# Kernel optimization log

Hardware: AMD Instinct MI355X
Metric: run time of the kernel (lower is better)

Reference implementation:

```python
import jax, jax.numpy as jnp
import numpy as np
import math

B, S, D, H = 2, 1024, 1024, 16
DH = D // H
BUCKETS, MAXPOS = 256, 512
SPAN = BUCKETS  # pos_ebd_size (att_span)


def make_log_bucket_position(rel, bucket_size, max_position):
    sign = jnp.sign(rel).astype(jnp.float32)
    mid = bucket_size // 2
    abs_pos = jnp.where((rel < mid) & (rel > -mid), mid - 1, jnp.abs(rel)).astype(jnp.float32)
    log_pos = jnp.ceil(jnp.log(abs_pos / mid) / np.log((max_position - 1) / mid) * (mid - 1)) + mid
    return jnp.where(abs_pos <= mid, rel.astype(jnp.float32), log_pos * sign).astype(jnp.int32)


def build_relative_position(q_size, k_size):
    rel = jnp.arange(q_size, dtype=jnp.int32)[:, None] - jnp.arange(k_size, dtype=jnp.int32)[None, :]
    return make_log_bucket_position(rel, BUCKETS, MAXPOS)


def setup_inputs() -> dict:
    key = jax.random.key(0)
    ks = jax.random.split(key, 8)
    w = lambda k: jax.random.normal(k, (D, D), dtype=jnp.float32) * 0.02
    return {
        "hidden_states": jax.random.normal(ks[0], (B, S, D), dtype=jnp.float32),
        "attention_mask": jnp.ones((B, 1, S, S), dtype=jnp.int32),
        "rel_embeddings": jax.random.normal(ks[1], (2 * SPAN, D), dtype=jnp.float32),
        "Wq": w(ks[2]), "bq": jnp.zeros((D,), jnp.float32),
        "Wk": w(ks[3]), "bk": jnp.zeros((D,), jnp.float32),
        "Wv": w(ks[4]), "bv": jnp.zeros((D,), jnp.float32),
    }


def reference(hidden_states, attention_mask, rel_embeddings, Wq, bq, Wk, bk, Wv, bv):
    split = lambda x: x.reshape(B, -1, H, DH).transpose(0, 2, 1, 3)  # [B,H,S,dh]
    q = split(hidden_states @ Wq + bq)
    k = split(hidden_states @ Wk + bk)
    v = split(hidden_states @ Wv + bv)

    SCALE_FACTOR = 3  # 1 + c2p + p2c
    scale = math.sqrt(DH * SCALE_FACTOR)
    scores = jnp.einsum('bhqd,bhkd->bhqk', q, k) / scale

    # disentangled relative-position bias (share_att_key=True -> reuse q/k proj)
    re = rel_embeddings[: 2 * SPAN]  # [2*SPAN, D]
    pos_q = (re @ Wq + bq).reshape(2 * SPAN, H, DH).transpose(1, 0, 2)  # [H,P,dh]
    pos_k = (re @ Wk + bk).reshape(2 * SPAN, H, DH).transpose(1, 0, 2)

    rel_pos = build_relative_position(S, S)  # [S,S] bucketized

    # c2p: gather along the position axis per (q,k) pair
    c2p_pos = jnp.clip(rel_pos + SPAN, 0, 2 * SPAN - 1)
    c2p_att = jnp.einsum('bhqd,hpd->bhqp', q, pos_k)  # [B,H,S,2*SPAN]
    c2p = jnp.take_along_axis(c2p_att, c2p_pos[None, None], axis=-1)  # [B,H,S,S]

    # p2c: gather for key positions, then transpose back to [q,k]
    p2c_pos = jnp.clip(-rel_pos + SPAN, 0, 2 * SPAN - 1)
    p2c_att = jnp.einsum('bhkd,hpd->bhkp', k, pos_q)
    p2c = jnp.swapaxes(jnp.take_along_axis(p2c_att, p2c_pos[None, None], axis=-1), -1, -2)

    scores = scores + (c2p + p2c) / scale

    # XSoftmax: masked fill -> softmax -> zero masked
    valid = attention_mask.astype(bool)
    scores = jnp.where(valid, scores, jnp.finfo(scores.dtype).min)
    probs = jax.nn.softmax(scores, axis=-1)
    probs = jnp.where(valid, probs, 0.0)

    ctx = jnp.einsum('bhqk,bhkd->bhqd', probs, v)
    return ctx.transpose(0, 2, 1, 3).reshape(B, S, D)
```

## Files before the change

### kernel.cpp

```cpp
#include <hip/hip_runtime.h>
#include <hip/hip_bf16.h>
#include <math.h>

#define B_   2
#define S_   1024
#define D_   1024
#define H_   16
#define DH_  64
#define P_   512

#define SCALE2 (0.07216878364870323f * 1.4426950408889634f)

typedef __bf16 bf16;
typedef __bf16 bf16x8 __attribute__((ext_vector_type(8)));
typedef __bf16 bf16x4 __attribute__((ext_vector_type(4)));
typedef float  f32x4  __attribute__((ext_vector_type(4)));

__device__ __forceinline__ f32x4 mfma16(bf16x8 a, bf16x8 b, f32x4 c) {
  return __builtin_amdgcn_mfma_f32_16x16x32_bf16(a, b, c, 0, 0, 0);
}

__device__ __forceinline__ bf16x8 ld8(const bf16* p) {
  return *reinterpret_cast<const bf16x8*>(p);
}

__device__ __forceinline__ void gl_lds16(const bf16* g, bf16* l) {
  __builtin_amdgcn_global_load_lds(
      (const __attribute__((address_space(1))) void*)g,
      (__attribute__((address_space(3))) void*)l, 16, 0, 0);
}

__device__ __forceinline__ bf16x8 ld8f(const float* p) {
  const f32x4* pv = reinterpret_cast<const f32x4*>(p);
  f32x4 lo = pv[0], hi = pv[1];
  bf16x8 r;
#pragma unroll
  for (int j = 0; j < 4; j++) { r[j] = (bf16)lo[j]; r[4 + j] = (bf16)hi[j]; }
  return r;
}

__global__ __launch_bounds__(256)
void k_convert(const float* __restrict__ hidden, const float* __restrict__ re,
               bf16* __restrict__ Xc, int* __restrict__ ci) {
  int gt = blockIdx.x * 256 + threadIdx.x;
  if (gt < 2047) {
    int rel = gt - 1023;
    int sgn = (rel > 0) - (rel < 0);
    float abs_pos = (rel < 128 && rel > -128) ? 127.0f : fabsf((float)rel);
    int bucket;
    if (abs_pos <= 128.0f) {
      bucket = rel;
    } else {
      const float logden = 1.3843393302355437f;
      float t1 = logf(abs_pos * (1.0f / 128.0f));
      float lp = ceilf(t1 / logden * 127.0f) + 128.0f;
      bucket = (int)lp * sgn;
    }
    ci[gt] = min(max(bucket + 256, 0), 511);
  }
  size_t i8 = (size_t)gt * 8;
  const size_t HN = (size_t)2048 * 1024;
  const float* src = (i8 < HN) ? (hidden + i8) : (re + (i8 - HN));
  *reinterpret_cast<bf16x8*>(&Xc[i8]) = ld8f(src);
}

__global__ __launch_bounds__(256)
void k_transpose(const float* __restrict__ Wq, const float* __restrict__ Wk,
                 const float* __restrict__ Wv, bf16* __restrict__ Wt) {
  __shared__ bf16 tile[64][72];
  const int t = threadIdx.x;
  const int w = blockIdx.z;
  const float* W = (w == 0) ? Wq : (w == 1) ? Wk : Wv;
  bf16* Out = Wt + (size_t)w * D_ * D_;
  const int k0 = blockIdx.y * 64;
  const int n0 = blockIdx.x * 64;
  {
    const int row = t >> 2, c0 = (t & 3) * 16;
    bf16x8 v0 = ld8f(W + (size_t)(k0 + row) * D_ + n0 + c0);
    bf16x8 v1 = ld8f(W + (size_t)(k0 + row) * D_ + n0 + c0 + 8);
    *reinterpret_cast<bf16x8*>(&tile[row][c0]) = v0;
    *reinterpret_cast<bf16x8*>(&tile[row][c0 + 8]) = v1;
  }
  __syncthreads();
  {
    const int nr = t >> 2, kc0 = (t & 3) * 16;
    bf16x8 o0, o1;
#pragma unroll
    for (int j = 0; j < 8; j++) o0[j] = tile[kc0 + j][nr];
#pragma unroll
    for (int j = 0; j < 8; j++) o1[j] = tile[kc0 + 8 + j][nr];
    *reinterpret_cast<bf16x8*>(&Out[(size_t)(n0 + nr) * D_ + k0 + kc0]) = o0;
    *reinterpret_cast<bf16x8*>(&Out[(size_t)(n0 + nr) * D_ + k0 + kc0 + 8]) = o1;
  }
}

__global__ __launch_bounds__(256)
void k_proj(const bf16* __restrict__ Xc, const bf16* __restrict__ Wt,
            const float* __restrict__ bq, const float* __restrict__ bk,
            const float* __restrict__ bv,
            bf16* __restrict__ qb, bf16* __restrict__ kb, bf16* __restrict__ vbT,
            bf16* __restrict__ posq, bf16* __restrict__ posk) {
  __shared__ bf16 As[128 * 64];
  __shared__ bf16 Bs[128 * 64];
  const int t = threadIdx.x;
  const int w = t >> 6, lane = t & 63, quad = lane >> 4, lc = lane & 15;
  const int wm = w >> 1, wn = w & 1;
  const int m0 = blockIdx.y * 128;
  const int wsel = blockIdx.x >> 3;
  const int n0 = (blockIdx.x & 7) * 128;
  const bf16* WtW = Wt + (size_t)wsel * D_ * D_;
  const float* bias = (wsel == 0) ? bq : (wsel == 1) ? bk : bv;
  const bf16* Agl = Xc + (size_t)m0 * D_;
  const bf16* Bgl = WtW + (size_t)n0 * D_;

  int rS[4], cS[4];
#pragma unroll
  for (int i = 0; i < 4; i++) {
    int g = i * 256 + t;
    rS[i] = g >> 3;
    cS[i] = (g & 7) ^ (rS[i] & 7);
  }

  f32x4 zv = {0.f, 0.f, 0.f, 0.f};
  f32x4 acc[4][4];
#pragma unroll
  for (int i = 0; i < 4; i++)
#pragma unroll
    for (int j = 0; j < 4; j++) acc[i][j] = zv;

  for (int k0 = 0; k0 < D_; k0 += 64) {
#pragma unroll
    for (int i = 0; i < 4; i++)
      gl_lds16(Agl + (size_t)rS[i] * D_ + k0 + cS[i] * 8,
               &As[(i * 256 + w * 64) * 8]);
#pragma unroll
    for (int i = 0; i < 4; i++)
      gl_lds16(Bgl + (size_t)rS[i] * D_ + k0 + cS[i] * 8,
               &Bs[(i * 256 + w * 64) * 8]);
    __syncthreads();

#pragma unroll
    for (int h = 0; h < 2; h++) {
      bf16x8 af[4], bfr[4];
#pragma unroll
      for (int mt = 0; mt < 4; mt++) {
        int row = wm * 64 + mt * 16 + lc;
        int ch = (h * 4 + quad) ^ (row & 7);
        af[mt] = ld8(&As[row * 64 + ch * 8]);
      }
#pragma unroll
      for (int nt = 0; nt < 4; nt++) {
        int row = wn * 64 + nt * 16 + lc;
        int ch = (h * 4 + quad) ^ (row & 7);
        bfr[nt] = ld8(&Bs[row * 64 + ch * 8]);
      }
#pragma unroll
      for (int mt = 0; mt < 4; mt++)
#pragma unroll
        for (int nt = 0; nt < 4; nt++)
          acc[mt][nt] = mfma16(af[mt], bfr[nt], acc[mt][nt]);
    }
    __syncthreads();
  }

#pragma unroll
  for (int nt = 0; nt < 4; nt++) {
    int nl = n0 + wn * 64 + nt * 16 + lc;
    float bsv = bias[nl];
    int h = nl >> 6, d = nl & 63;
    if (wsel == 2) {
#pragma unroll
      for (int mt = 0; mt < 4; mt++) {
        int i0 = m0 + wm * 64 + mt * 16 + quad * 4;
        if (i0 < 2048) {
          int b = i0 >> 10, s0 = i0 & 1023;
          bf16x4 ov;
#pragma unroll
          for (int r = 0; r < 4; r++) ov[r] = (bf16)(acc[mt][nt][r] + bsv);
          *reinterpret_cast<bf16x4*>(
              &vbT[(((size_t)(b * H_ + h)) * DH_ + d) * S_ + s0]) = ov;
        }
      }
    } else {
      bf16* dst = (wsel == 0) ? qb : kb;
#pragma unroll
      for (int mt = 0; mt < 4; mt++) {
#pragma unroll
        for (int r = 0; r < 4; r++) {
          int i = m0 + wm * 64 + mt * 16 + quad * 4 + r;
          bf16 ob = (bf16)(acc[mt][nt][r] + bsv);
          if (i < 2048) {
            int b = i >> 10, s = i & 1023;
            dst[(((size_t)(b * H_ + h)) * S_ + s) * DH_ + d] = ob;
          } else {
            int p = i - 2048;
            if (wsel == 0)      posq[((size_t)(h * P_ + p)) * DH_ + d] = ob;
            else                posk[((size_t)(h * P_ + p)) * DH_ + d] = ob;
          }
        }
      }
    }
  }
}

__global__ __launch_bounds__(256)
void k_rel(const bf16* __restrict__ qb, const bf16* __restrict__ kb,
           const bf16* __restrict__ posq, const bf16* __restrict__ posk,
           bf16* __restrict__ c2p, bf16* __restrict__ p2c) {
  const int t = threadIdx.x;
  const int w = t >> 6, lane = t & 63, quad = lane >> 4, lc = lane & 15;
  const int which = blockIdx.z & 1;
  const int bh = blockIdx.z >> 1;
  const int h = bh & (H_ - 1);
  const int q0 = blockIdx.x * 64;
  const bf16* QK = (which ? kb : qb) + (size_t)bh * S_ * DH_;
  const bf16* PM = (which ? posq : posk) + (size_t)h * P_ * DH_;
  bf16* Out = (which ? p2c : c2p) + (size_t)bh * S_ * P_;

  f32x4 zv = {0.f, 0.f, 0.f, 0.f};
  bf16x8 bq[4][2];
#pragma unroll
  for (int qi = 0; qi < 4; qi++) {
    const bf16* qp = QK + (size_t)(q0 + qi * 16 + lc) * DH_ + quad * 8;
    bq[qi][0] = ld8(qp);
    bq[qi][1] = ld8(qp + 32);
  }
  const int p0 = w * 128;
#pragma unroll 2
  for (int pt = 0; pt < 8; pt++) {
    const bf16* pp = PM + (size_t)(p0 + pt * 16 + lc) * DH_ + quad * 8;
    bf16x8 pa0 = ld8(pp), pa1 = ld8(pp + 32);
#pragma unroll
    for (int qi = 0; qi < 4; qi++) {
      f32x4 acc = mfma16(pa1, bq[qi][1], mfma16(pa0, bq[qi][0], zv));
      int q = q0 + qi * 16 + lc;
      int pbase = p0 + pt * 16 + quad * 4;
      bf16x4 ov;
#pragma unroll
      for (int r = 0; r < 4; r++) ov[r] = (bf16)acc[r];
      *reinterpret_cast<bf16x4*>(&Out[(size_t)q * P_ + pbase]) = ov;
    }
  }
}

__global__ __launch_bounds__(256)
void k_attn(const bf16* __restrict__ qb, const bf16* __restrict__ kb,
            const bf16* __restrict__ vbT, const bf16* __restrict__ c2p,
            const bf16* __restrict__ p2c, const int* __restrict__ citab,
            float* __restrict__ out) {
  __shared__ bf16 c2pS[64 * 136];
  __shared__ bf16 p2cS[64 * 136];
  __shared__ bf16 vT[64 * 64];
  __shared__ bf16 Pld[4][16][72];
  __shared__ int  ciS[128];

  const int t = threadIdx.x;
  const int w = t >> 6, lane = t & 63, quad = lane >> 4, lc = lane & 15;
  const int bh = blockIdx.x;
  const int q0 = blockIdx.y * 64;
  const int qw = q0 + w * 16;

  const bf16* qp = qb + ((size_t)bh * S_ + qw + lc) * DH_ + quad * 8;
  bf16x8 aq0 = ld8(qp), aq1 = ld8(qp + 32);

  const bf16* kbB = kb + (size_t)bh * S_ * DH_;
  const bf16* vbB = vbT + (size_t)bh * DH_ * S_;
  const bf16* c2pB = c2p + (size_t)bh * S_ * P_;
  const bf16* p2cB = p2c + (size_t)bh * S_ * P_;

  int wrow[5], wch[5];
#pragma unroll
  for (int i = 0; i < 5; i++) {
    int slot = i * 256 + ((i == 4) ? (t & 63) : t);
    wrow[i] = slot / 17;
    wch[i] = slot - wrow[i] * 17;
  }
  int vrow[2], vch[2];
#pragma unroll
  for (int i = 0; i < 2; i++) {
    int slot = i * 256 + t;
    vrow[i] = slot >> 3;
    vch[i] = (slot & 7) ^ (vrow[i] & 7);
  }

  f32x4 zv = {0.f, 0.f, 0.f, 0.f};
  float m_r[4], l_r[4];
  f32x4 oacc[4];
#pragma unroll
  for (int r = 0; r < 4; r++) { m_r[r] = -INFINITY; l_r[r] = 0.f; }
#pragma unroll
  for (int dg = 0; dg < 4; dg++) oacc[dg] = zv;

  for (int kt = 0; kt < S_; kt += 64) {
    const int clo8 = citab[q0 - kt - 63 + 1023] & ~7;

    bf16x8 kf[4][2];
#pragma unroll
    for (int g = 0; g < 4; g++) {
      const bf16* kp = kbB + (size_t)(kt + g * 16 + lc) * DH_ + quad * 8;
      kf[g][0] = ld8(kp);
      kf[g][1] = ld8(kp + 32);
    }

    if (t < 127) ciS[t] = citab[q0 - kt - 63 + 1023 + t];

#pragma unroll
    for (int i = 0; i < 4; i++) {
      gl_lds16(c2pB + (size_t)(q0 + wrow[i]) * P_ + clo8 + wch[i] * 8,
               &c2pS[(i * 256 + w * 64) * 8]);
      gl_lds16(p2cB + (size_t)(kt + wrow[i]) * P_ + clo8 + wch[i] * 8,
               &p2cS[(i * 256 + w * 64) * 8]);
    }
    if (w == 0) {
      gl_lds16(c2pB + (size_t)(q0 + wrow[4]) * P_ + clo8 + wch[4] * 8,
               &c2pS[1024 * 8]);
      gl_lds16(p2cB + (size_t)(kt + wrow[4]) * P_ + clo8 + wch[4] * 8,
               &p2cS[1024 * 8]);
    }
#pragma unroll
    for (int i = 0; i < 2; i++)
      gl_lds16(vbB + (size_t)vrow[i] * S_ + kt + vch[i] * 8,
               &vT[(i * 256 + w * 64) * 8]);

    f32x4 s[4];
#pragma unroll
    for (int g = 0; g < 4; g++)
      s[g] = mfma16(aq1, kf[g][1], mfma16(aq0, kf[g][0], zv));

    __syncthreads();

#pragma unroll
    for (int g = 0; g < 4; g++) {
      int kc = g * 16 + lc;
#pragma unroll
      for (int r = 0; r < 4; r++) {
        int qr = w * 16 + quad * 4 + r;
        int j = ciS[qr - kc + 63] - clo8;
        float cv = (float)c2pS[qr * 136 + j];
        float pv = (float)p2cS[kc * 136 + j];
        s[g][r] = (s[g][r] + cv + pv) * SCALE2;
      }
    }
#pragma unroll
    for (int r = 0; r < 4; r++) {
      float mx = fmaxf(fmaxf(s[0][r], s[1][r]), fmaxf(s[2][r], s[3][r]));
#pragma unroll
      for (int o2 = 1; o2 < 16; o2 <<= 1) mx = fmaxf(mx, __shfl_xor(mx, o2, 16));
      float mnew = fmaxf(m_r[r], mx);
      float alpha = exp2f(m_r[r] - mnew);
      m_r[r] = mnew;
      float ps = 0.f;
#pragma unroll
      for (int g = 0; g < 4; g++) {
        float pe = exp2f(s[g][r] - mnew);
        s[g][r] = pe;
        ps += pe;
      }
#pragma unroll
      for (int o2 = 1; o2 < 16; o2 <<= 1) ps += __shfl_xor(ps, o2, 16);
      l_r[r] = l_r[r] * alpha + ps;
#pragma unroll
      for (int dg = 0; dg < 4; dg++) oacc[dg][r] *= alpha;
    }
#pragma unroll
    for (int g = 0; g < 4; g++)
#pragma unroll
      for (int r = 0; r < 4; r++)
        Pld[w][quad * 4 + r][g * 16 + lc] = (bf16)s[g][r];

    bf16x8 ap0 = *reinterpret_cast<bf16x8*>(&Pld[w][lc][quad * 8]);
    bf16x8 ap1 = *reinterpret_cast<bf16x8*>(&Pld[w][lc][32 + quad * 8]);
#pragma unroll
    for (int dg = 0; dg < 4; dg++) {
      int row = dg * 16 + lc;
      bf16x8 bv0 = ld8(&vT[row * 64 + (quad ^ (row & 7)) * 8]);
      bf16x8 bv1 = ld8(&vT[row * 64 + ((quad + 4) ^ (row & 7)) * 8]);
      oacc[dg] = mfma16(ap1, bv1, mfma16(ap0, bv0, oacc[dg]));
    }
    __syncthreads();
  }

  const int b = bh >> 4, h = bh & 15;
#pragma unroll
  for (int r = 0; r < 4; r++) {
    float inv = 1.0f / l_r[r];
    int qa = qw + quad * 4 + r;
#pragma unroll
    for (int dg = 0; dg < 4; dg++)
      out[((size_t)(b * S_) + qa) * D_ + h * DH_ + dg * 16 + lc] =
          oacc[dg][r] * inv;
  }
}

extern "C" void kernel_launch(void* const* d_in, const int* in_sizes, int n_in,
                              void* d_out, int out_size, void* d_ws,
                              size_t ws_size, hipStream_t stream) {
  const float* hidden = (const float*)d_in[0];
  const float* re = (const float*)d_in[2];
  const float* Wq = (const float*)d_in[3];
  const float* bq = (const float*)d_in[4];
  const float* Wk = (const float*)d_in[5];
  const float* bk = (const float*)d_in[6];
  const float* Wv = (const float*)d_in[7];
  const float* bv = (const float*)d_in[8];

  char* ws = (char*)d_ws;
  const size_t MB = 1024 * 1024;
  bf16* qb   = (bf16*)(ws + 0 * MB);
  bf16* kb   = (bf16*)(ws + 4 * MB);
  bf16* vbT  = (bf16*)(ws + 8 * MB);
  bf16* posq = (bf16*)(ws + 12 * MB);
  bf16* posk = (bf16*)(ws + 13 * MB);
  int*  ci   = (int*) (ws + 14 * MB);
  bf16* Wt   = (bf16*)(ws + 15 * MB);
  bf16* c2p  = (bf16*)(ws + 26 * MB);
  bf16* p2c  = (bf16*)(ws + 58 * MB);
  bf16* Xc   = (bf16*)(ws + 26 * MB);
  if (ws_size < 92 * MB) return;

  k_convert<<<dim3(1280), dim3(256), 0, stream>>>(hidden, re, Xc, ci);
  k_transpose<<<dim3(16, 16, 3), dim3(256), 0, stream>>>(Wq, Wk, Wv, Wt);
  k_proj<<<dim3(24, 20), dim3(256), 0, stream>>>(Xc, Wt, bq, bk, bv,
                                                 qb, kb, vbT, posq, posk);
  k_rel<<<dim3(16, 1, 64), dim3(256), 0, stream>>>(qb, kb, posq, posk, c2p, p2c);
  k_attn<<<dim3(32, 16), dim3(256), 0, stream>>>(qb, kb, vbT, c2p, p2c, ci,
                                                 (float*)d_out);
}
```

Baseline: 220.6 us.

## Split attention key range across two blocks and merge with combine kernel

The attention kernel now splits the key dimension into two halves along a new grid z axis. Each half writes its unnormalized partial output and its per-row (max, sum) pair. A new combine kernel rescales the two partials and normalizes them. This doubles the grid from 512 to 1024 blocks to fill more compute units, at the cost of an extra kernel launch and extra partial-output traffic. The po1 buffer reuses the Wt workspace region, which is safe only because Wt is no longer needed after projection.

```diff
diff --git a/kernel.cpp b/kernel.cpp
--- a/kernel.cpp
+++ b/kernel.cpp
@@ -247,7 +247,8 @@
 void k_attn(const bf16* __restrict__ qb, const bf16* __restrict__ kb,
             const bf16* __restrict__ vbT, const bf16* __restrict__ c2p,
             const bf16* __restrict__ p2c, const int* __restrict__ citab,
-            float* __restrict__ out) {
+            float* __restrict__ out, float* __restrict__ po1,
+            float2* __restrict__ ml) {
   __shared__ bf16 c2pS[64 * 136];
   __shared__ bf16 p2cS[64 * 136];
   __shared__ bf16 vT[64 * 64];
@@ -258,6 +259,8 @@
   const int w = t >> 6, lane = t & 63, quad = lane >> 4, lc = lane & 15;
   const int bh = blockIdx.x;
   const int q0 = blockIdx.y * 64;
+  const int ks = blockIdx.z;
+  const int ktlo = ks * 512;
   const int qw = q0 + w * 16;
 
   const bf16* qp = qb + ((size_t)bh * S_ + qw + lc) * DH_ + quad * 8;
@@ -291,7 +294,7 @@
 #pragma unroll
   for (int dg = 0; dg < 4; dg++) oacc[dg] = zv;
 
-  for (int kt = 0; kt < S_; kt += 64) {
+  for (int kt = ktlo; kt < ktlo + 512; kt += 64) {
     const int clo8 = citab[q0 - kt - 63 + 1023] & ~7;
 
     bf16x8 kf[4][2];
@@ -381,15 +384,38 @@
   }
 
   const int b = bh >> 4, h = bh & 15;
+  float* od = (ks == 0) ? out : po1;
 #pragma unroll
   for (int r = 0; r < 4; r++) {
-    float inv = 1.0f / l_r[r];
     int qa = qw + quad * 4 + r;
 #pragma unroll
     for (int dg = 0; dg < 4; dg++)
-      out[((size_t)(b * S_) + qa) * D_ + h * DH_ + dg * 16 + lc] =
-          oacc[dg][r] * inv;
-  }
+      od[((size_t)(b * S_) + qa) * D_ + h * DH_ + dg * 16 + lc] = oacc[dg][r];
+    if (lc == 0)
+      ml[((size_t)(ks * 32 + bh)) * S_ + qa] = make_float2(m_r[r], l_r[r]);
+  }
+}
+
+__global__ __launch_bounds__(256)
+void k_combine(float* __restrict__ out, const float* __restrict__ po1,
+               const float2* __restrict__ ml) {
+  size_t e = ((size_t)blockIdx.x * 256 + threadIdx.x) * 4;
+  int row = (int)(e >> 10);
+  int hd  = (int)(e & 1023);
+  int b = row >> 10, s = row & 1023;
+  int bh = b * H_ + (hd >> 6);
+  size_t mr = (size_t)bh * S_ + s;
+  float2 p0 = ml[mr];
+  float2 p1 = ml[(size_t)32 * S_ + mr];
+  float m = fmaxf(p0.x, p1.x);
+  float a0 = exp2f(p0.x - m), a1 = exp2f(p1.x - m);
+  float inv = 1.0f / (p0.y * a0 + p1.y * a1);
+  f32x4 v0 = *reinterpret_cast<const f32x4*>(&out[e]);
+  f32x4 v1 = *reinterpret_cast<const f32x4*>(&po1[e]);
+  f32x4 rr;
+#pragma unroll
+  for (int j = 0; j < 4; j++) rr[j] = (v0[j] * a0 + v1[j] * a1) * inv;
+  *reinterpret_cast<f32x4*>(&out[e]) = rr;
 }
 
 extern "C" void kernel_launch(void* const* d_in, const int* in_sizes, int n_in,
@@ -416,6 +442,8 @@
   bf16* c2p  = (bf16*)(ws + 26 * MB);
   bf16* p2c  = (bf16*)(ws + 58 * MB);
   bf16* Xc   = (bf16*)(ws + 26 * MB);
+  float*  po1 = (float*) (ws + 15 * MB);
+  float2* ml  = (float2*)(ws + 23 * MB);
   if (ws_size < 92 * MB) return;
 
   k_convert<<<dim3(1280), dim3(256), 0, stream>>>(hidden, re, Xc, ci);
@@ -423,6 +451,7 @@
   k_proj<<<dim3(24, 20), dim3(256), 0, stream>>>(Xc, Wt, bq, bk, bv,
                                                  qb, kb, vbT, posq, posk);
   k_rel<<<dim3(16, 1, 64), dim3(256), 0, stream>>>(qb, kb, posq, posk, c2p, p2c);
-  k_attn<<<dim3(32, 16), dim3(256), 0, stream>>>(qb, kb, vbT, c2p, p2c, ci,
-                                                 (float*)d_out);
-}
+  k_attn<<<dim3(32, 16, 2), dim3(256), 0, stream>>>(qb, kb, vbT, c2p, p2c, ci,
+                                                    (float*)d_out, po1, ml);
+  k_combine<<<dim3(2048), dim3(256), 0, stream>>>((float*)d_out, po1, ml);
+}
```

Measured after the change: 230.2 us. 1.04x slower.
